# Kernel tuning notes

Measured on AMD Instinct MI355X. Metric: run time of the kernel, lower is better.

The kernel has to match this reference:

```python
import jax, jax.numpy as jnp
import numpy as np

N = 100000      # num_nodes
E = 1600000     # num_edges
IN_DIM = 6
EDGE_DIM = 2
H = 5           # heads
C = 5           # out_channels per head (hidden_dim)
D = H * C       # 25, hidden width
L = 3           # num_layers
INV_SQRT_C = np.float32(1.0 / np.sqrt(C))


def setup_inputs() -> dict:
    key = jax.random.key(0)
    ks = jax.random.split(key, 18)
    s = 0.1
    inp = {
        "x": jax.random.normal(ks[0], (N, IN_DIM), dtype=jnp.float32),
        "edge_index": jax.random.randint(ks[1], (2, E), 0, N, dtype=jnp.int64),
        "edge_attr": jax.random.normal(ks[2], (E, EDGE_DIM), dtype=jnp.float32),
        # input projection
        "Wi": jax.random.normal(ks[3], (IN_DIM, D), dtype=jnp.float32) * s,
        "bi": jnp.zeros((D,), dtype=jnp.float32),
        # per-layer TransformerConv params, stacked over layers
        "Wq": jax.random.normal(ks[4], (L, D, D), dtype=jnp.float32) * s,
        "bq": jnp.zeros((L, D), dtype=jnp.float32),
        "Wk": jax.random.normal(ks[5], (L, D, D), dtype=jnp.float32) * s,
        "bk": jnp.zeros((L, D), dtype=jnp.float32),
        "Wv": jax.random.normal(ks[6], (L, D, D), dtype=jnp.float32) * s,
        "bv": jnp.zeros((L, D), dtype=jnp.float32),
        "We": jax.random.normal(ks[7], (L, EDGE_DIM, D), dtype=jnp.float32) * s,  # lin_edge, no bias
        "Wskip": jax.random.normal(ks[8], (L, D, D), dtype=jnp.float32) * s,
        "bskip": jnp.zeros((L, D), dtype=jnp.float32),
        # output head
        "Wo": jax.random.normal(ks[9], (D, 1), dtype=jnp.float32) * s,
        "bo": jnp.zeros((1,), dtype=jnp.float32),
    }
    return inp


def _forward(x, edge_index, edge_attr, Wi, bi, Wq, bq, Wk, bk, Wv, bv, We, Wskip, bskip, Wo, bo):
    src, dst = edge_index[0], edge_index[1]
    h = x @ Wi + bi  # [N, D]
    for l in range(L):
        q = (h @ Wq[l] + bq[l]).reshape(N, H, C)
        k = (h @ Wk[l] + bk[l]).reshape(N, H, C)
        v = (h @ Wv[l] + bv[l]).reshape(N, H, C)
        e = (edge_attr @ We[l]).reshape(E, H, C)  # per-edge projection
        k_j = k[src] + e                           # [E, H, C]
        alpha = jnp.einsum('ehc,ehc->eh', q[dst], k_j) * INV_SQRT_C  # [E, H]
        # scatter-softmax over destination neighborhoods (PyG softmax)
        amax = jax.ops.segment_max(alpha, dst, num_segments=N)       # [N, H]
        ex = jnp.exp(alpha - amax[dst])
        denom = jax.ops.segment_sum(ex, dst, num_segments=N)         # [N, H]
        alpha = ex / (denom[dst] + 1e-16)
        msg = (v[src] + e) * alpha[:, :, None]                       # [E, H, C]
        out = jax.ops.segment_sum(msg, dst, num_segments=N).reshape(N, D)
        h = out + h @ Wskip[l] + bskip[l]          # root_weight skip
    return jax.nn.sigmoid(h @ Wo + bo)             # [N, 1]


def reference(x, edge_index, edge_attr, Wi, bi, Wq, bq, Wk, bk, Wv, bv, We, Wskip, bskip, Wo, bo):
    return _forward(x, edge_index, edge_attr, Wi, bi, Wq, bq, Wk, bk, Wv, bv, We, Wskip, bskip, Wo, bo)
```

## Files before the change

kernel.cpp:

```cpp
#include <hip/hip_runtime.h>
#include <hip/hip_bf16.h>
#include <math.h>

#define NN 100000
#define NE 1600000
#define IN_DIM 6
#define EDGE_DIM 2
#define HH 5
#define CC 5
#define DD 25
#define DS 32
#define INV_SQRT_C 0.4472135954999579f
#define NBUK 200
#define BUKW 500
#define CAP 10000
#define KPB 800
#define CH (NE / KPB)
#define NPB 48
#define NBLK ((NN + NPB - 1) / NPB)
#define NBD ((NN + 255) / 256)
#define CSTR 16


__device__ __forceinline__ unsigned int f2bf(float f) {
    unsigned int u = __float_as_uint(f);
    return (u + 0x7fffu + ((u >> 16) & 1u)) >> 16;
}
__device__ __forceinline__ float bflo(unsigned int u) { return __uint_as_float(u << 16); }
__device__ __forceinline__ float bfhi(unsigned int u) { return __uint_as_float(u & 0xffff0000u); }

__global__ __launch_bounds__(256) void k_part(const int* __restrict__ ei,
                                              const float* __restrict__ ea,
                                              int* __restrict__ cursor,
                                              uint2* __restrict__ slab) {
    __shared__ int sdst[CH];
    __shared__ int scnt[NBUK];
    __shared__ int sbase[NBUK];
    __shared__ int swp[NBUK];
    int base = blockIdx.x * CH;
    for (int i = threadIdx.x; i < NBUK; i += 256) scnt[i] = 0;
    __syncthreads();
    for (int i = threadIdx.x; i < CH; i += 256) {
        int dst = ei[NE + base + i];
        sdst[i] = dst;
        atomicAdd(&scnt[dst / BUKW], 1);
    }
    __syncthreads();
    for (int i = threadIdx.x; i < NBUK; i += 256) {
        sbase[i] = i * CAP + atomicAdd(&cursor[i * CSTR], scnt[i]);
        swp[i] = 0;
    }
    __syncthreads();
    for (int i = threadIdx.x; i < CH; i += 256) {
        int dst = sdst[i];
        int b = dst / BUKW;
        int src = ei[base + i];
        float2 eav = ((const float2*)ea)[base + i];
        int p = sbase[b] + atomicAdd(&swp[b], 1);
        uint2 r;
        r.x = (unsigned)src | ((unsigned)(dst - b * BUKW) << 17);
        r.y = f2bf(eav.x) | (f2bf(eav.y) << 16);
        slab[p] = r;
    }
}

__global__ __launch_bounds__(512) void k_place(const int* __restrict__ cursor,
                                               const uint2* __restrict__ slab,
                                               int* __restrict__ rowptr,
                                               uint2* __restrict__ csr) {
    __shared__ int hist[BUKW];
    __shared__ int cur[BUKW];
    __shared__ int s[512];
    int b = blockIdx.x;
    int t = threadIdx.x;
    int node0 = b * BUKW;
    int begin = b * CAP;
    int cnt = cursor[b * CSTR];
    s[t] = (t < NBUK && t < b) ? cursor[t * CSTR] : 0;
    __syncthreads();
    for (int off = 256; off > 0; off >>= 1) {
        if (t < off) s[t] += s[t + off];
        __syncthreads();
    }
    int bOff = s[0];
    __syncthreads();
    for (int i = t; i < BUKW; i += 512) hist[i] = 0;
    __syncthreads();
    for (int i = t; i < cnt; i += 512) {
        uint2 r = slab[begin + i];
        atomicAdd(&hist[r.x >> 17], 1);
    }
    __syncthreads();
    int hv = (t < BUKW) ? hist[t] : 0;
    s[t] = hv;
    __syncthreads();
    for (int off = 1; off < 512; off <<= 1) {
        int u = (t >= off) ? s[t - off] : 0;
        __syncthreads();
        s[t] += u;
        __syncthreads();
    }
    if (t < BUKW) {
        int o = bOff + s[t] - hv;
        rowptr[node0 + t] = o;
        cur[t] = o;
    }
    if (b == NBUK - 1 && t == 0) rowptr[NN] = NE;
    __syncthreads();
    for (int i = t; i < cnt; i += 512) {
        uint2 r = slab[begin + i];
        int dl = (int)(r.x >> 17);
        int p = atomicAdd(&cur[dl], 1);
        uint2 o;
        o.x = r.x & 0x1FFFFu;
        o.y = r.y;
        csr[p] = o;
    }
}

__global__ void k_dh(const int* __restrict__ rowptr, int* __restrict__ bhist) {
    __shared__ int lh[256];
    int t = threadIdx.x;
    lh[t] = 0;
    __syncthreads();
    int i = blockIdx.x * 256 + t;
    if (i < NN) {
        int d = rowptr[i + 1] - rowptr[i];
        atomicAdd(&lh[d > 255 ? 255 : d], 1);
    }
    __syncthreads();
    bhist[t * NBD + blockIdx.x] = lh[t];
}

__global__ __launch_bounds__(512) void k_ds(int* __restrict__ bhist, int* __restrict__ binTot) {
    __shared__ int s[512];
    int bin = blockIdx.x;
    int t = threadIdx.x;
    int v = (t < NBD) ? bhist[bin * NBD + t] : 0;
    s[t] = v;
    __syncthreads();
    for (int off = 1; off < 512; off <<= 1) {
        int u = (t >= off) ? s[t - off] : 0;
        __syncthreads();
        s[t] += u;
        __syncthreads();
    }
    if (t < NBD) bhist[bin * NBD + t] = s[t] - v;
    if (t == 511) binTot[bin] = s[511];
}

__global__ void k_ds2(int* __restrict__ binTot, int* __restrict__ binOff) {
    __shared__ int s[256];
    int t = threadIdx.x;
    int v = binTot[t];
    s[t] = v;
    __syncthreads();
    for (int off = 1; off < 256; off <<= 1) {
        int u = (t >= off) ? s[t - off] : 0;
        __syncthreads();
        s[t] += u;
        __syncthreads();
    }
    binOff[t] = s[t] - v;
}

__global__ void k_dp(const int* __restrict__ rowptr, const int* __restrict__ bhist,
                     const int* __restrict__ binOff, int* __restrict__ perm) {
    __shared__ int lcur[256];
    int t = threadIdx.x;
    lcur[t] = 0;
    __syncthreads();
    int i = blockIdx.x * 256 + t;
    if (i < NN) {
        int d = rowptr[i + 1] - rowptr[i];
        if (d > 255) d = 255;
        int r = atomicAdd(&lcur[d], 1);
        int pos = binOff[d] + bhist[d * NBD + blockIdx.x] + r;
        perm[NN - 1 - pos] = i;
    }
}

__global__ void k_input_proj(const float* __restrict__ x, const float* __restrict__ Wi,
                             const float* __restrict__ bi, float* __restrict__ h) {
    __shared__ float sW[IN_DIM * DD];
    __shared__ float sb[DD];
    int t = threadIdx.x;
    if (t < IN_DIM * DD) sW[t] = Wi[t];
    if (t < DD) sb[t] = bi[t];
    __syncthreads();
    int tid = blockIdx.x * blockDim.x + t;
    int n = tid / DD, d = tid - n * DD;
    if (n >= NN) return;
    float acc = sb[d];
    const float* xr = x + n * IN_DIM;
#pragma unroll
    for (int i = 0; i < IN_DIM; i++) acc += xr[i] * sW[i * DD + d];
    h[n * DS + d] = acc;
}

__global__ void k_qkv_skip(const float* __restrict__ h,
                           const float* __restrict__ Wq, const float* __restrict__ bq,
                           const float* __restrict__ Wk, const float* __restrict__ bk,
                           const float* __restrict__ Wv, const float* __restrict__ bv,
                           const float* __restrict__ Ws, const float* __restrict__ bs,
                           __hip_bfloat16* __restrict__ q, __hip_bfloat16* __restrict__ kv,
                           float* __restrict__ hout) {
    __shared__ float sWq[DD * DD], sWk[DD * DD], sWv[DD * DD], sWs[DD * DD];
    __shared__ float sb[4 * DD];
    for (int i = threadIdx.x; i < DD * DD; i += blockDim.x) {
        sWq[i] = Wq[i]; sWk[i] = Wk[i]; sWv[i] = Wv[i]; sWs[i] = Ws[i];
    }
    if (threadIdx.x < DD) {
        sb[threadIdx.x]          = bq[threadIdx.x];
        sb[DD + threadIdx.x]     = bk[threadIdx.x];
        sb[2 * DD + threadIdx.x] = bv[threadIdx.x];
        sb[3 * DD + threadIdx.x] = bs[threadIdx.x];
    }
    __syncthreads();
    int tid = blockIdx.x * blockDim.x + threadIdx.x;
    int n = tid / DD, d = tid - n * DD;
    if (n >= NN) return;
    float aq = sb[d], ak = sb[DD + d], av = sb[2 * DD + d], asv = sb[3 * DD + d];
    const float* hr = h + (size_t)n * DS;
#pragma unroll
    for (int i = 0; i < DD; i++) {
        float hv = hr[i];
        aq  += hv * sWq[i * DD + d];
        ak  += hv * sWk[i * DD + d];
        av  += hv * sWv[i * DD + d];
        asv += hv * sWs[i * DD + d];
    }
    int h5 = d / 5, c5 = d - 5 * h5;
    q[(size_t)n * 40 + 8 * h5 + c5] = __float2bfloat16(aq * INV_SQRT_C);
    size_t rb = (size_t)n * 64;
    kv[rb + 8 * h5 + c5] = __float2bfloat16(ak);
    if (c5 < 3) kv[rb + 8 * h5 + 5 + c5] = __float2bfloat16(av);
    else        kv[rb + 40 + 2 * h5 + (c5 - 3)] = __float2bfloat16(av);
    hout[(size_t)n * DS + d] = asv;
}

struct EState { float l, Sx, Sy, a0, a1, a2, a3, a4; };

__device__ __forceinline__ void edge_acc(EState& st, uint2 rec, uint4 A, unsigned int B,
                                         float qa0, float qa1, float qa2, float qa3, float qa4,
                                         float qwx, float qwy) {
    float eax = bflo(rec.y), eay = bfhi(rec.y);
    float k0 = bflo(A.x), k1 = bfhi(A.x), k2 = bflo(A.y), k3 = bfhi(A.y), k4 = bflo(A.z);
    float v0 = bfhi(A.z), v1 = bflo(A.w), v2 = bfhi(A.w), v3 = bflo(B), v4 = bfhi(B);
    float s = qa0 * k0 + qa1 * k1 + qa2 * k2 + qa3 * k3 + qa4 * k4 + eax * qwx + eay * qwy;
    float cf = __expf(s);
    st.l += cf; st.Sx += cf * eax; st.Sy += cf * eay;
    st.a0 += cf * v0; st.a1 += cf * v1; st.a2 += cf * v2; st.a3 += cf * v3; st.a4 += cf * v4;
}

__global__ __launch_bounds__(256) void k_edge_fused(
    const int* __restrict__ rowptr, const uint2* __restrict__ csr,
    const int* __restrict__ perm,
    const float* __restrict__ We, const __hip_bfloat16* __restrict__ q,
    const __hip_bfloat16* __restrict__ kv, float* __restrict__ hout,
    int fuse_head, const float* __restrict__ Wo, const float* __restrict__ bo,
    float* __restrict__ out) {
    __shared__ float sWe[EDGE_DIM * DD];
    __shared__ float sWo[DD];
    __shared__ float sbo;
    if (threadIdx.x < EDGE_DIM * DD) sWe[threadIdx.x] = We[threadIdx.x];
    if (threadIdx.x < DD) sWo[threadIdx.x] = Wo[threadIdx.x];
    if (threadIdx.x == 0) sbo = bo[0];
    __syncthreads();
    int lane = threadIdx.x & 63;
    int wv   = threadIdx.x >> 6;
    int grp  = lane / 5;
    int h    = lane - grp * 5;
    int idx  = blockIdx.x * NPB + wv * 12 + grp;
    bool act = (grp < 12) && (idx < NN);
    int node = 0;

    int beg = 0, end = 0;
    float qa0 = 0, qa1 = 0, qa2 = 0, qa3 = 0, qa4 = 0, qwx = 0, qwy = 0;
    if (act) {
        node = perm[idx];
        beg = rowptr[node];
        end = rowptr[node + 1];
        uint4 qc = *(const uint4*)(q + (size_t)node * 40 + 8 * h);
        qa0 = bflo(qc.x); qa1 = bfhi(qc.x); qa2 = bflo(qc.y); qa3 = bfhi(qc.y); qa4 = bflo(qc.z);
        const float* wx = &sWe[5 * h];
        const float* wy = &sWe[DD + 5 * h];
        qwx = qa0 * wx[0] + qa1 * wx[1] + qa2 * wx[2] + qa3 * wx[3] + qa4 * wx[4];
        qwy = qa0 * wy[0] + qa1 * wy[1] + qa2 * wy[2] + qa3 * wy[3] + qa4 * wy[4];
    }

    EState st = {0.f, 0.f, 0.f, 0.f, 0.f, 0.f, 0.f, 0.f};

    int p = beg;
    for (; p + 4 <= end; p += 4) {
        uint2 r0 = csr[p], r1 = csr[p + 1], r2 = csr[p + 2], r3 = csr[p + 3];
        const __hip_bfloat16* b0 = kv + ((size_t)r0.x << 6);
        const __hip_bfloat16* b1 = kv + ((size_t)r1.x << 6);
        const __hip_bfloat16* b2 = kv + ((size_t)r2.x << 6);
        const __hip_bfloat16* b3 = kv + ((size_t)r3.x << 6);
        uint4 A0 = *(const uint4*)(b0 + 8 * h);
        uint4 A1 = *(const uint4*)(b1 + 8 * h);
        uint4 A2 = *(const uint4*)(b2 + 8 * h);
        uint4 A3 = *(const uint4*)(b3 + 8 * h);
        unsigned int B0 = *(const unsigned int*)(b0 + 40 + 2 * h);
        unsigned int B1 = *(const unsigned int*)(b1 + 40 + 2 * h);
        unsigned int B2 = *(const unsigned int*)(b2 + 40 + 2 * h);
        unsigned int B3 = *(const unsigned int*)(b3 + 40 + 2 * h);
        edge_acc(st, r0, A0, B0, qa0, qa1, qa2, qa3, qa4, qwx, qwy);
        edge_acc(st, r1, A1, B1, qa0, qa1, qa2, qa3, qa4, qwx, qwy);
        edge_acc(st, r2, A2, B2, qa0, qa1, qa2, qa3, qa4, qwx, qwy);
        edge_acc(st, r3, A3, B3, qa0, qa1, qa2, qa3, qa4, qwx, qwy);
    }
    for (; p < end; ++p) {
        uint2 r0 = csr[p];
        const __hip_bfloat16* b0 = kv + ((size_t)r0.x << 6);
        uint4 A0 = *(const uint4*)(b0 + 8 * h);
        unsigned int B0 = *(const unsigned int*)(b0 + 40 + 2 * h);
        edge_acc(st, r0, A0, B0, qa0, qa1, qa2, qa3, qa4, qwx, qwy);
    }

    float dot = 0.f;
    if (act) {
        float inv = 1.0f / (st.l + 1e-16f);
        const float* wx = &sWe[5 * h];
        const float* wy = &sWe[DD + 5 * h];
        float* ho = hout + (size_t)node * DS + 5 * h;
        float n0 = ho[0] + (st.a0 + st.Sx * wx[0] + st.Sy * wy[0]) * inv;
        float n1 = ho[1] + (st.a1 + st.Sx * wx[1] + st.Sy * wy[1]) * inv;
        float n2 = ho[2] + (st.a2 + st.Sx * wx[2] + st.Sy * wy[2]) * inv;
        float n3 = ho[3] + (st.a3 + st.Sx * wx[3] + st.Sy * wy[3]) * inv;
        float n4 = ho[4] + (st.a4 + st.Sx * wx[4] + st.Sy * wy[4]) * inv;
        ho[0] = n0; ho[1] = n1; ho[2] = n2; ho[3] = n3; ho[4] = n4;
        if (fuse_head) {
            const float* wo = &sWo[5 * h];
            dot = n0 * wo[0] + n1 * wo[1] + n2 * wo[2] + n3 * wo[3] + n4 * wo[4];
        }
    }
    if (fuse_head) {
        float dsum = dot;
#pragma unroll
        for (int k = 1; k < 5; k++) dsum += __shfl(dot, (grp * 5 + k) & 63, 64);
        if (act && h == 0) out[node] = 1.0f / (1.0f + __expf(-(dsum + sbo)));
    }
}

extern "C" void kernel_launch(void* const* d_in, const int* in_sizes, int n_in,
                              void* d_out, int out_size, void* d_ws, size_t ws_size,
                              hipStream_t stream) {
    const float* x     = (const float*)d_in[0];
    const int*   ei    = (const int*)d_in[1];
    const float* ea    = (const float*)d_in[2];
    const float* Wi    = (const float*)d_in[3];
    const float* bi    = (const float*)d_in[4];
    const float* Wq    = (const float*)d_in[5];
    const float* bq    = (const float*)d_in[6];
    const float* Wk    = (const float*)d_in[7];
    const float* bk    = (const float*)d_in[8];
    const float* Wv    = (const float*)d_in[9];
    const float* bv    = (const float*)d_in[10];
    const float* We    = (const float*)d_in[11];
    const float* Wskip = (const float*)d_in[12];
    const float* bskip = (const float*)d_in[13];
    const float* Wo    = (const float*)d_in[14];
    const float* bo    = (const float*)d_in[15];
    float* out = (float*)d_out;
    (void)in_sizes; (void)n_in; (void)out_size; (void)ws_size;

    char* wsb = (char*)d_ws;
    size_t off = 0;
    auto alloc = [&](size_t bytes) {
        void* p = wsb + off;
        off += (bytes + 127) & ~(size_t)127;
        return p;
    };
    uint2* slab   = (uint2*)alloc((size_t)NBUK * CAP * sizeof(uint2));
    uint2* csr    = (uint2*)alloc((size_t)NE * sizeof(uint2));
    __hip_bfloat16* kvrec = (__hip_bfloat16*)alloc((size_t)NN * 64 * 2);
    __hip_bfloat16* qrec  = (__hip_bfloat16*)alloc((size_t)NN * 40 * 2);
    float* hA     = (float*)alloc((size_t)NN * DS * sizeof(float));
    float* hB     = (float*)alloc((size_t)NN * DS * sizeof(float));
    int*   rowptr = (int*)alloc((size_t)(NN + 1) * sizeof(int));
    int*   cursor = (int*)alloc((size_t)NBUK * CSTR * sizeof(int));
    int*   bhist  = (int*)alloc((size_t)256 * NBD * sizeof(int));
    int*   binTot = (int*)alloc(256 * sizeof(int));
    int*   binOff = (int*)alloc(256 * sizeof(int));
    int*   perm   = (int*)alloc((size_t)NN * sizeof(int));

    dim3 blk(256);
    int gND = (NN * DD + 255) / 256;

    (void)hipMemsetAsync(cursor, 0, (size_t)NBUK * CSTR * sizeof(int), stream);
    k_part<<<KPB, blk, 0, stream>>>(ei, ea, cursor, slab);
    k_place<<<NBUK, dim3(512), 0, stream>>>(cursor, slab, rowptr, csr);
    k_dh<<<NBD, blk, 0, stream>>>(rowptr, bhist);
    k_ds<<<256, dim3(512), 0, stream>>>(bhist, binTot);
    k_ds2<<<1, blk, 0, stream>>>(binTot, binOff);
    k_dp<<<NBD, blk, 0, stream>>>(rowptr, bhist, binOff, perm);

    k_input_proj<<<gND, blk, 0, stream>>>(x, Wi, bi, hA);

    float* hc = hA;
    float* hn = hB;
    for (int l = 0; l < 3; l++) {
        k_qkv_skip<<<gND, blk, 0, stream>>>(hc,
                                            Wq + (size_t)l * DD * DD, bq + (size_t)l * DD,
                                            Wk + (size_t)l * DD * DD, bk + (size_t)l * DD,
                                            Wv + (size_t)l * DD * DD, bv + (size_t)l * DD,
                                            Wskip + (size_t)l * DD * DD, bskip + (size_t)l * DD,
                                            qrec, kvrec, hn);
        k_edge_fused<<<NBLK, blk, 0, stream>>>(rowptr, csr, perm,
                                               We + (size_t)l * EDGE_DIM * DD,
                                               qrec, kvrec, hn,
                                               (l == 2) ? 1 : 0, Wo, bo, out);
        float* t = hc; hc = hn; hn = t;
    }
}
```

Before: 360.4 us.

## Replace atomic slab partition with deterministic count-scan CSR build and fuse preprocessing

The global-atomic bucket partition with fixed-capacity slabs becomes a count / scan / scatter pipeline that writes into a compact staging buffer. The degree histogram is folded into k_place, which removes the k_dh kernel. k_dp now also emits per-slot begin/end pairs so the edge kernel reads them directly instead of doing dependent rowptr lookups. The input projection is fused into the first-layer qkv kernel, which drops a launch and an h write/read, at the cost of recomputing x@Wi per output thread and adding extra small launches elsewhere.

```diff
diff --git a/kernel.cpp b/kernel.cpp
--- a/kernel.cpp
+++ b/kernel.cpp
@@ -13,13 +13,10 @@
 #define INV_SQRT_C 0.4472135954999579f
 #define NBUK 200
 #define BUKW 500
-#define CAP 10000
 #define KPB 800
 #define CH (NE / KPB)
 #define NPB 48
 #define NBLK ((NN + NPB - 1) / NPB)
-#define NBD ((NN + 255) / 256)
-#define CSTR 16
 
 
 __device__ __forceinline__ unsigned int f2bf(float f) {
@@ -29,27 +26,67 @@
 __device__ __forceinline__ float bflo(unsigned int u) { return __uint_as_float(u << 16); }
 __device__ __forceinline__ float bfhi(unsigned int u) { return __uint_as_float(u & 0xffff0000u); }
 
-__global__ __launch_bounds__(256) void k_part(const int* __restrict__ ei,
-                                              const float* __restrict__ ea,
-                                              int* __restrict__ cursor,
-                                              uint2* __restrict__ slab) {
+__global__ __launch_bounds__(256) void k_cnt(const int* __restrict__ ei, int* __restrict__ cnt) {
+    __shared__ int scnt[NBUK];
+    int base = blockIdx.x * CH;
+    for (int i = threadIdx.x; i < NBUK; i += 256) scnt[i] = 0;
+    __syncthreads();
+    for (int i = threadIdx.x; i < CH; i += 256)
+        atomicAdd(&scnt[ei[NE + base + i] / BUKW], 1);
+    __syncthreads();
+    for (int i = threadIdx.x; i < NBUK; i += 256)
+        cnt[blockIdx.x * NBUK + i] = scnt[i];
+}
+
+__global__ __launch_bounds__(1024) void k_cscan(const int* __restrict__ cnt,
+                                                int* __restrict__ off,
+                                                int* __restrict__ bucketTot) {
+    __shared__ int s[1024];
+    int b = blockIdx.x;
+    int t = threadIdx.x;
+    int v = (t < KPB) ? cnt[t * NBUK + b] : 0;
+    s[t] = v;
+    __syncthreads();
+    for (int o = 1; o < 1024; o <<= 1) {
+        int u = (t >= o) ? s[t - o] : 0;
+        __syncthreads();
+        s[t] += u;
+        __syncthreads();
+    }
+    if (t < KPB) off[b * KPB + t] = s[t] - v;
+    if (t == 1023) bucketTot[b] = s[1023];
+}
+
+__global__ void k_bscan(const int* __restrict__ bucketTot, int* __restrict__ bucketBase) {
+    __shared__ int s[256];
+    int t = threadIdx.x;
+    int v = (t < NBUK) ? bucketTot[t] : 0;
+    s[t] = v;
+    __syncthreads();
+    for (int o = 1; o < 256; o <<= 1) {
+        int u = (t >= o) ? s[t - o] : 0;
+        __syncthreads();
+        s[t] += u;
+        __syncthreads();
+    }
+    if (t < NBUK) bucketBase[t] = s[t] - v;
+}
+
+__global__ __launch_bounds__(256) void k_part2(const int* __restrict__ ei,
+                                               const float* __restrict__ ea,
+                                               const int* __restrict__ off,
+                                               const int* __restrict__ bucketBase,
+                                               uint2* __restrict__ stage) {
     __shared__ int sdst[CH];
-    __shared__ int scnt[NBUK];
     __shared__ int sbase[NBUK];
     __shared__ int swp[NBUK];
-    int base = blockIdx.x * CH;
-    for (int i = threadIdx.x; i < NBUK; i += 256) scnt[i] = 0;
-    __syncthreads();
-    for (int i = threadIdx.x; i < CH; i += 256) {
-        int dst = ei[NE + base + i];
-        sdst[i] = dst;
-        atomicAdd(&scnt[dst / BUKW], 1);
-    }
-    __syncthreads();
+    int blk = blockIdx.x;
+    int base = blk * CH;
     for (int i = threadIdx.x; i < NBUK; i += 256) {
-        sbase[i] = i * CAP + atomicAdd(&cursor[i * CSTR], scnt[i]);
+        sbase[i] = bucketBase[i] + off[i * KPB + blk];
         swp[i] = 0;
     }
+    for (int i = threadIdx.x; i < CH; i += 256) sdst[i] = ei[NE + base + i];
     __syncthreads();
     for (int i = threadIdx.x; i < CH; i += 256) {
         int dst = sdst[i];
@@ -60,55 +97,54 @@
         uint2 r;
         r.x = (unsigned)src | ((unsigned)(dst - b * BUKW) << 17);
         r.y = f2bf(eav.x) | (f2bf(eav.y) << 16);
-        slab[p] = r;
-    }
-}
-
-__global__ __launch_bounds__(512) void k_place(const int* __restrict__ cursor,
-                                               const uint2* __restrict__ slab,
+        stage[p] = r;
+    }
+}
+
+__global__ __launch_bounds__(512) void k_place(const int* __restrict__ bucketTot,
+                                               const int* __restrict__ bucketBase,
+                                               const uint2* __restrict__ stage,
                                                int* __restrict__ rowptr,
-                                               uint2* __restrict__ csr) {
+                                               uint2* __restrict__ csr,
+                                               int* __restrict__ dbh) {
     __shared__ int hist[BUKW];
     __shared__ int cur[BUKW];
     __shared__ int s[512];
+    __shared__ int lh[256];
     int b = blockIdx.x;
     int t = threadIdx.x;
     int node0 = b * BUKW;
-    int begin = b * CAP;
-    int cnt = cursor[b * CSTR];
-    s[t] = (t < NBUK && t < b) ? cursor[t * CSTR] : 0;
-    __syncthreads();
-    for (int off = 256; off > 0; off >>= 1) {
-        if (t < off) s[t] += s[t + off];
-        __syncthreads();
-    }
-    int bOff = s[0];
-    __syncthreads();
+    int begin = b == 0 ? 0 : 0;
+    begin = bucketBase[b];
+    int cnt = bucketTot[b];
     for (int i = t; i < BUKW; i += 512) hist[i] = 0;
+    if (t < 256) lh[t] = 0;
     __syncthreads();
     for (int i = t; i < cnt; i += 512) {
-        uint2 r = slab[begin + i];
+        uint2 r = stage[begin + i];
         atomicAdd(&hist[r.x >> 17], 1);
     }
     __syncthreads();
     int hv = (t < BUKW) ? hist[t] : 0;
     s[t] = hv;
     __syncthreads();
-    for (int off = 1; off < 512; off <<= 1) {
-        int u = (t >= off) ? s[t - off] : 0;
+    for (int o = 1; o < 512; o <<= 1) {
+        int u = (t >= o) ? s[t - o] : 0;
         __syncthreads();
         s[t] += u;
         __syncthreads();
     }
     if (t < BUKW) {
-        int o = bOff + s[t] - hv;
+        int o = begin + s[t] - hv;
         rowptr[node0 + t] = o;
         cur[t] = o;
+        atomicAdd(&lh[hv > 255 ? 255 : hv], 1);
     }
     if (b == NBUK - 1 && t == 0) rowptr[NN] = NE;
     __syncthreads();
+    if (t < 256) dbh[b * 256 + t] = lh[t];
     for (int i = t; i < cnt; i += 512) {
-        uint2 r = slab[begin + i];
+        uint2 r = stage[begin + i];
         int dl = (int)(r.x >> 17);
         int p = atomicAdd(&cur[dl], 1);
         uint2 o;
@@ -118,45 +154,32 @@
     }
 }
 
-__global__ void k_dh(const int* __restrict__ rowptr, int* __restrict__ bhist) {
-    __shared__ int lh[256];
-    int t = threadIdx.x;
-    lh[t] = 0;
-    __syncthreads();
-    int i = blockIdx.x * 256 + t;
-    if (i < NN) {
-        int d = rowptr[i + 1] - rowptr[i];
-        atomicAdd(&lh[d > 255 ? 255 : d], 1);
-    }
-    __syncthreads();
-    bhist[t * NBD + blockIdx.x] = lh[t];
-}
-
-__global__ __launch_bounds__(512) void k_ds(int* __restrict__ bhist, int* __restrict__ binTot) {
-    __shared__ int s[512];
+__global__ void k_ds(const int* __restrict__ dbh, int* __restrict__ dbhE,
+                     int* __restrict__ binTot) {
+    __shared__ int s[256];
     int bin = blockIdx.x;
     int t = threadIdx.x;
-    int v = (t < NBD) ? bhist[bin * NBD + t] : 0;
+    int v = (t < NBUK) ? dbh[t * 256 + bin] : 0;
     s[t] = v;
     __syncthreads();
-    for (int off = 1; off < 512; off <<= 1) {
-        int u = (t >= off) ? s[t - off] : 0;
+    for (int o = 1; o < 256; o <<= 1) {
+        int u = (t >= o) ? s[t - o] : 0;
         __syncthreads();
         s[t] += u;
         __syncthreads();
     }
-    if (t < NBD) bhist[bin * NBD + t] = s[t] - v;
-    if (t == 511) binTot[bin] = s[511];
-}
-
-__global__ void k_ds2(int* __restrict__ binTot, int* __restrict__ binOff) {
+    if (t < NBUK) dbhE[bin * NBUK + t] = s[t] - v;
+    if (t == 255) binTot[bin] = s[255];
+}
+
+__global__ void k_ds2(const int* __restrict__ binTot, int* __restrict__ binOff) {
     __shared__ int s[256];
     int t = threadIdx.x;
     int v = binTot[t];
     s[t] = v;
     __syncthreads();
-    for (int off = 1; off < 256; off <<= 1) {
-        int u = (t >= off) ? s[t - off] : 0;
+    for (int o = 1; o < 256; o <<= 1) {
+        int u = (t >= o) ? s[t - o] : 0;
         __syncthreads();
         s[t] += u;
         __syncthreads();
@@ -164,41 +187,32 @@
     binOff[t] = s[t] - v;
 }
 
-__global__ void k_dp(const int* __restrict__ rowptr, const int* __restrict__ bhist,
-                     const int* __restrict__ binOff, int* __restrict__ perm) {
+__global__ __launch_bounds__(512) void k_dp(const int* __restrict__ rowptr,
+                                            const int* __restrict__ dbhE,
+                                            const int* __restrict__ binOff,
+                                            int* __restrict__ perm,
+                                            uint2* __restrict__ begend) {
     __shared__ int lcur[256];
-    int t = threadIdx.x;
-    lcur[t] = 0;
-    __syncthreads();
-    int i = blockIdx.x * 256 + t;
-    if (i < NN) {
-        int d = rowptr[i + 1] - rowptr[i];
+    int b = blockIdx.x;
+    int t = threadIdx.x;
+    if (t < 256) lcur[t] = 0;
+    __syncthreads();
+    if (t < BUKW) {
+        int node = b * BUKW + t;
+        int beg = rowptr[node], end = rowptr[node + 1];
+        int d = end - beg;
         if (d > 255) d = 255;
         int r = atomicAdd(&lcur[d], 1);
-        int pos = binOff[d] + bhist[d * NBD + blockIdx.x] + r;
-        perm[NN - 1 - pos] = i;
-    }
-}
-
-__global__ void k_input_proj(const float* __restrict__ x, const float* __restrict__ Wi,
-                             const float* __restrict__ bi, float* __restrict__ h) {
-    __shared__ float sW[IN_DIM * DD];
-    __shared__ float sb[DD];
-    int t = threadIdx.x;
-    if (t < IN_DIM * DD) sW[t] = Wi[t];
-    if (t < DD) sb[t] = bi[t];
-    __syncthreads();
-    int tid = blockIdx.x * blockDim.x + t;
-    int n = tid / DD, d = tid - n * DD;
-    if (n >= NN) return;
-    float acc = sb[d];
-    const float* xr = x + n * IN_DIM;
-#pragma unroll
-    for (int i = 0; i < IN_DIM; i++) acc += xr[i] * sW[i * DD + d];
-    h[n * DS + d] = acc;
+        int pos = binOff[d] + dbhE[d * NBUK + b] + r;
+        int slot = NN - 1 - pos;
+        perm[slot] = node;
+        begend[slot] = make_uint2((unsigned)beg, (unsigned)end);
+    }
 }
 
 __global__ void k_qkv_skip(const float* __restrict__ h,
+                           const float* __restrict__ x, const float* __restrict__ WiC,
+                           const float* __restrict__ biC, int use_x,
                            const float* __restrict__ Wq, const float* __restrict__ bq,
                            const float* __restrict__ Wk, const float* __restrict__ bk,
                            const float* __restrict__ Wv, const float* __restrict__ bv,
@@ -206,25 +220,42 @@
                            __hip_bfloat16* __restrict__ q, __hip_bfloat16* __restrict__ kv,
                            float* __restrict__ hout) {
     __shared__ float sWq[DD * DD], sWk[DD * DD], sWv[DD * DD], sWs[DD * DD];
+    __shared__ float sWi[IN_DIM * DD];
     __shared__ float sb[4 * DD];
+    __shared__ float sbi[DD];
     for (int i = threadIdx.x; i < DD * DD; i += blockDim.x) {
         sWq[i] = Wq[i]; sWk[i] = Wk[i]; sWv[i] = Wv[i]; sWs[i] = Ws[i];
     }
+    if (use_x && threadIdx.x < IN_DIM * DD) sWi[threadIdx.x] = WiC[threadIdx.x];
     if (threadIdx.x < DD) {
         sb[threadIdx.x]          = bq[threadIdx.x];
         sb[DD + threadIdx.x]     = bk[threadIdx.x];
         sb[2 * DD + threadIdx.x] = bv[threadIdx.x];
         sb[3 * DD + threadIdx.x] = bs[threadIdx.x];
+        if (use_x) sbi[threadIdx.x] = biC[threadIdx.x];
     }
     __syncthreads();
     int tid = blockIdx.x * blockDim.x + threadIdx.x;
     int n = tid / DD, d = tid - n * DD;
     if (n >= NN) return;
     float aq = sb[d], ak = sb[DD + d], av = sb[2 * DD + d], asv = sb[3 * DD + d];
+    float xr[IN_DIM];
     const float* hr = h + (size_t)n * DS;
+    if (use_x) {
+        const float* xp = x + (size_t)n * IN_DIM;
+#pragma unroll
+        for (int j = 0; j < IN_DIM; j++) xr[j] = xp[j];
+    }
 #pragma unroll
     for (int i = 0; i < DD; i++) {
-        float hv = hr[i];
+        float hv;
+        if (use_x) {
+            hv = sbi[i];
+#pragma unroll
+            for (int j = 0; j < IN_DIM; j++) hv += xr[j] * sWi[j * DD + i];
+        } else {
+            hv = hr[i];
+        }
         aq  += hv * sWq[i * DD + d];
         ak  += hv * sWk[i * DD + d];
         av  += hv * sWv[i * DD + d];
@@ -254,7 +285,7 @@
 }
 
 __global__ __launch_bounds__(256) void k_edge_fused(
-    const int* __restrict__ rowptr, const uint2* __restrict__ csr,
+    const uint2* __restrict__ begend, const uint2* __restrict__ csr,
     const int* __restrict__ perm,
     const float* __restrict__ We, const __hip_bfloat16* __restrict__ q,
     const __hip_bfloat16* __restrict__ kv, float* __restrict__ hout,
@@ -279,8 +310,8 @@
     float qa0 = 0, qa1 = 0, qa2 = 0, qa3 = 0, qa4 = 0, qwx = 0, qwy = 0;
     if (act) {
         node = perm[idx];
-        beg = rowptr[node];
-        end = rowptr[node + 1];
+        uint2 be = begend[idx];
+        beg = (int)be.x; end = (int)be.y;
         uint4 qc = *(const uint4*)(q + (size_t)node * 40 + 8 * h);
         qa0 = bflo(qc.x); qa1 = bfhi(qc.x); qa2 = bflo(qc.y); qa3 = bfhi(qc.y); qa4 = bflo(qc.z);
         const float* wx = &sWe[5 * h];
@@ -367,48 +398,52 @@
     (void)in_sizes; (void)n_in; (void)out_size; (void)ws_size;
 
     char* wsb = (char*)d_ws;
-    size_t off = 0;
+    size_t off0 = 0;
     auto alloc = [&](size_t bytes) {
-        void* p = wsb + off;
-        off += (bytes + 127) & ~(size_t)127;
+        void* p = wsb + off0;
+        off0 += (bytes + 127) & ~(size_t)127;
         return p;
     };
-    uint2* slab   = (uint2*)alloc((size_t)NBUK * CAP * sizeof(uint2));
+    uint2* stage  = (uint2*)alloc((size_t)NE * sizeof(uint2));
     uint2* csr    = (uint2*)alloc((size_t)NE * sizeof(uint2));
     __hip_bfloat16* kvrec = (__hip_bfloat16*)alloc((size_t)NN * 64 * 2);
     __hip_bfloat16* qrec  = (__hip_bfloat16*)alloc((size_t)NN * 40 * 2);
     float* hA     = (float*)alloc((size_t)NN * DS * sizeof(float));
     float* hB     = (float*)alloc((size_t)NN * DS * sizeof(float));
     int*   rowptr = (int*)alloc((size_t)(NN + 1) * sizeof(int));
-    int*   cursor = (int*)alloc((size_t)NBUK * CSTR * sizeof(int));
-    int*   bhist  = (int*)alloc((size_t)256 * NBD * sizeof(int));
+    int*   cnt    = (int*)alloc((size_t)KPB * NBUK * sizeof(int));
+    int*   offm   = (int*)alloc((size_t)NBUK * KPB * sizeof(int));
+    int*   bucketTot  = (int*)alloc(NBUK * sizeof(int));
+    int*   bucketBase = (int*)alloc(NBUK * sizeof(int));
+    int*   dbh    = (int*)alloc((size_t)NBUK * 256 * sizeof(int));
+    int*   dbhE   = (int*)alloc((size_t)256 * NBUK * sizeof(int));
     int*   binTot = (int*)alloc(256 * sizeof(int));
     int*   binOff = (int*)alloc(256 * sizeof(int));
     int*   perm   = (int*)alloc((size_t)NN * sizeof(int));
+    uint2* begend = (uint2*)alloc((size_t)NN * sizeof(uint2));
 
     dim3 blk(256);
     int gND = (NN * DD + 255) / 256;
 
-    (void)hipMemsetAsync(cursor, 0, (size_t)NBUK * CSTR * sizeof(int), stream);
-    k_part<<<KPB, blk, 0, stream>>>(ei, ea, cursor, slab);
-    k_place<<<NBUK, dim3(512), 0, stream>>>(cursor, slab, rowptr, csr);
-    k_dh<<<NBD, blk, 0, stream>>>(rowptr, bhist);
-    k_ds<<<256, dim3(512), 0, stream>>>(bhist, binTot);
+    k_cnt<<<KPB, blk, 0, stream>>>(ei, cnt);
+    k_cscan<<<NBUK, dim3(1024), 0, stream>>>(cnt, offm, bucketTot);
+    k_bscan<<<1, blk, 0, stream>>>(bucketTot, bucketBase);
+    k_part2<<<KPB, blk, 0, stream>>>(ei, ea, offm, bucketBase, stage);
+    k_place<<<NBUK, dim3(512), 0, stream>>>(bucketTot, bucketBase, stage, rowptr, csr, dbh);
+    k_ds<<<256, blk, 0, stream>>>(dbh, dbhE, binTot);
     k_ds2<<<1, blk, 0, stream>>>(binTot, binOff);
-    k_dp<<<NBD, blk, 0, stream>>>(rowptr, bhist, binOff, perm);
-
-    k_input_proj<<<gND, blk, 0, stream>>>(x, Wi, bi, hA);
+    k_dp<<<NBUK, dim3(512), 0, stream>>>(rowptr, dbhE, binOff, perm, begend);
 
     float* hc = hA;
     float* hn = hB;
     for (int l = 0; l < 3; l++) {
-        k_qkv_skip<<<gND, blk, 0, stream>>>(hc,
+        k_qkv_skip<<<gND, blk, 0, stream>>>(hc, x, Wi, bi, (l == 0) ? 1 : 0,
                                             Wq + (size_t)l * DD * DD, bq + (size_t)l * DD,
                                             Wk + (size_t)l * DD * DD, bk + (size_t)l * DD,
                                             Wv + (size_t)l * DD * DD, bv + (size_t)l * DD,
                                             Wskip + (size_t)l * DD * DD, bskip + (size_t)l * DD,
                                             qrec, kvrec, hn);
-        k_edge_fused<<<NBLK, blk, 0, stream>>>(rowptr, csr, perm,
+        k_edge_fused<<<NBLK, blk, 0, stream>>>(begend, csr, perm,
                                                We + (size_t)l * EDGE_DIM * DD,
                                                qrec, kvrec, hn,
                                                (l == 2) ? 1 : 0, Wo, bo, out);
```

Measured after the change: 502.0 us. 39.3% more time.
